# Kernel optimization log

Hardware: AMD Instinct MI355X
Metric: run time of the kernel (lower is better)

The kernel has to match this reference:

```python
import jax, jax.numpy as jnp
import numpy as np

N_NODES = 100000
N_EDGES = 1600000
D_IN = 128
D_H = 128          # hidden_channels * heads (heads=1)
N_LAYERS = 5
N_GRAPHS = 64
N_TARGETS = 1
EPS = 1e-5
NEG_SLOPE = 0.2    # PyG GATConv leaky_relu default


def setup_inputs() -> dict:
    key = jax.random.key(0)
    ks = jax.random.split(key, 16)
    x = jax.random.normal(ks[0], (N_NODES, D_IN), dtype=jnp.float32)
    edge_index = jax.random.randint(ks[1], (2, N_EDGES), 0, N_NODES, dtype=jnp.int32)
    batch = jnp.sort(jax.random.randint(ks[2], (N_NODES,), 0, N_GRAPHS, dtype=jnp.int32))
    s = 1.0 / np.sqrt(D_H)
    W = jax.random.normal(ks[3], (N_LAYERS, D_IN, D_H), dtype=jnp.float32) * s
    a_src = jax.random.normal(ks[4], (N_LAYERS, D_H), dtype=jnp.float32) * s
    a_dst = jax.random.normal(ks[5], (N_LAYERS, D_H), dtype=jnp.float32) * s
    b = jax.random.normal(ks[6], (N_LAYERS, D_H), dtype=jnp.float32) * 0.01
    bn_gamma = jnp.ones((N_LAYERS, D_H), dtype=jnp.float32) + 0.1 * jax.random.normal(ks[7], (N_LAYERS, D_H), dtype=jnp.float32)
    bn_beta = 0.1 * jax.random.normal(ks[8], (N_LAYERS, D_H), dtype=jnp.float32)
    bn_mean = 0.1 * jax.random.normal(ks[9], (N_LAYERS, D_H), dtype=jnp.float32)
    bn_var = jax.random.uniform(ks[10], (N_LAYERS, D_H), dtype=jnp.float32, minval=0.5, maxval=1.5)
    lin_w = jax.random.normal(ks[11], (D_H, N_TARGETS), dtype=jnp.float32) * s
    lin_b = jnp.zeros((N_TARGETS,), dtype=jnp.float32)
    return {"x": x, "edge_index": edge_index, "batch": batch, "W": W,
            "a_src": a_src, "a_dst": a_dst, "b": b,
            "bn_gamma": bn_gamma, "bn_beta": bn_beta, "bn_mean": bn_mean,
            "bn_var": bn_var, "lin_w": lin_w, "lin_b": lin_b}


def _gat_layer(h, src, dst, W, a_s, a_d, bias):
    # PyG GATConv (heads=1): linear transform, per-edge attention, softmax over
    # incoming edges of each destination node, weighted sum aggregation.
    xp = h @ W                                   # [N, C]
    s_node = xp @ a_s                            # [N]
    d_node = xp @ a_d                            # [N]
    e = jax.nn.leaky_relu(s_node[src] + d_node[dst], NEG_SLOPE)   # [E]
    m = jax.ops.segment_max(e, dst, num_segments=N_NODES)         # [N]
    w = jnp.exp(e - m[dst])                                       # [E]
    denom = jax.ops.segment_sum(w, dst, num_segments=N_NODES)     # [N] (>0: self-loops)
    alpha = w / denom[dst]                                        # [E]
    out = jax.ops.segment_sum(alpha[:, None] * xp[src], dst, num_segments=N_NODES)
    return out + bias


def reference(x, edge_index, batch, W, a_src, a_dst, b,
              bn_gamma, bn_beta, bn_mean, bn_var, lin_w, lin_b):
    # add self-loops (PyG GATConv default add_self_loops=True)
    loops = jnp.arange(N_NODES, dtype=edge_index.dtype)
    src = jnp.concatenate([edge_index[0], loops])
    dst = jnp.concatenate([edge_index[1], loops])
    h = x
    for l in range(N_LAYERS):
        h = _gat_layer(h, src, dst, W[l], a_src[l], a_dst[l], b[l])
        h = jax.nn.relu(h)
        # dropout: identity (eval mode); BatchNorm1d in eval mode (running stats)
        h = (h - bn_mean[l]) * (bn_gamma[l] / jnp.sqrt(bn_var[l] + EPS)) + bn_beta[l]
    # global mean pool over graphs
    sums = jax.ops.segment_sum(h, batch, num_segments=N_GRAPHS)            # [G, C]
    cnt = jax.ops.segment_sum(jnp.ones((N_NODES,), h.dtype), batch, num_segments=N_GRAPHS)
    g = sums / jnp.maximum(cnt, 1.0)[:, None]
    return g @ lin_w + lin_b
```

## Files before the change

### kernel.cpp

```cpp
#include <hip/hip_runtime.h>
#include <hip/hip_fp16.h>
#include <math.h>


#define NN 100000
#define NE 1600000
#define DH 128
#define NL 5
#define NG 64

static constexpr int ET = NE + NN;
static constexpr int NBK = (NN + 255) >> 8;
static constexpr int CAP = 6144;

typedef __attribute__((ext_vector_type(8))) _Float16 f16x8;
typedef __attribute__((ext_vector_type(4))) float f32x4;
typedef __attribute__((ext_vector_type(2))) float f32x2;

__device__ __forceinline__ unsigned short f2h(float v) {
    __half h = __float2half(v);
    return *reinterpret_cast<unsigned short*>(&h);
}
__device__ __forceinline__ float h2f(unsigned short u) {
    __half h = *reinterpret_cast<__half*>(&u);
    return __half2float(h);
}


__global__ __launch_bounds__(256) void k_wprep(const float* __restrict__ W,
                                               unsigned short* __restrict__ wtg) {
    int i = blockIdx.x * 256 + threadIdx.x;
    if (i >= NL * DH * DH) return;
    int l = i >> 14, rem = i & 16383;
    int k = rem >> 7, c = rem & 127;
    wtg[(l << 14) + (c << 7) + k] = f2h(W[i]);
}

__global__ __launch_bounds__(256) void k_bnprep(const float* __restrict__ ga,
                                                const float* __restrict__ be,
                                                const float* __restrict__ me,
                                                const float* __restrict__ va,
                                                float* __restrict__ g2,
                                                float* __restrict__ b2) {
    int i = blockIdx.x * 256 + threadIdx.x;
    if (i < NL * DH) {
        float s = ga[i] * rsqrtf(va[i] + 1e-5f);
        g2[i] = s;
        b2[i] = be[i] - me[i] * s;
    }
}

__global__ __launch_bounds__(256) void k_cnt(const int* __restrict__ batch,
                                             int* __restrict__ cnts) {
    __shared__ int hc[NG];
    int t = threadIdx.x;
    if (t < NG) hc[t] = 0;
    __syncthreads();
    int base = blockIdx.x * 4096;
#pragma unroll
    for (int k = 0; k < 16; ++k) {
        int i = base + k * 256 + t;
        if (i < NN) atomicAdd(&hc[batch[i]], 1);
    }
    __syncthreads();
    if (t < NG && hc[t]) atomicAdd(&cnts[t], hc[t]);
}


__global__ __launch_bounds__(512) void k_bscatter(const int* __restrict__ src,
                                                  const int* __restrict__ dst,
                                                  int* __restrict__ bcnt,
                                                  int* __restrict__ pairs) {
    __shared__ int lcnt[NBK];
    __shared__ int lbase[NBK];
    for (int i = threadIdx.x; i < NBK; i += 512) lcnt[i] = 0;
    __syncthreads();
    int base = blockIdx.x * 4096;
    int es[8], ed[8], er[8];
#pragma unroll
    for (int k = 0; k < 8; ++k) {
        int i = base + k * 512 + threadIdx.x;
        if (i < ET) {
            int s, d;
            if (i < NE) { s = src[i]; d = dst[i]; } else { s = d = i - NE; }
            es[k] = s; ed[k] = d;
            er[k] = atomicAdd(&lcnt[d >> 8], 1);
        } else {
            ed[k] = -1;
        }
    }
    __syncthreads();
    for (int i = threadIdx.x; i < NBK; i += 512)
        lbase[i] = lcnt[i] ? atomicAdd(&bcnt[i], lcnt[i]) : 0;
    __syncthreads();
#pragma unroll
    for (int k = 0; k < 8; ++k) {
        if (ed[k] >= 0) {
            int bk = ed[k] >> 8;
            pairs[(size_t)bk * CAP + lbase[bk] + er[k]] =
                es[k] | ((ed[k] & 255) << 17);
        }
    }
}

__global__ __launch_bounds__(512) void k_bscan(const int* __restrict__ bcnt,
                                               int* __restrict__ bbase,
                                               int* __restrict__ row_ptr) {
    __shared__ int sm[512];
    int t = threadIdx.x;
    int v = (t < NBK) ? bcnt[t] : 0;
    sm[t] = v;
    __syncthreads();
    for (int off = 1; off < 512; off <<= 1) {
        int u = (t >= off) ? sm[t - off] : 0;
        __syncthreads();
        sm[t] += u;
        __syncthreads();
    }
    if (t < NBK) bbase[t] = sm[t] - v;
    if (t == 0) { bbase[NBK] = ET; row_ptr[NN] = ET; }
}

__global__ __launch_bounds__(256) void k_bfinal(const int* __restrict__ pairs,
                                                const int* __restrict__ bcnt,
                                                const int* __restrict__ bbase,
                                                int* __restrict__ row_ptr,
                                                int* __restrict__ csr_src) {
    __shared__ int ldeg[256];
    __shared__ int lcur[256];
    __shared__ int sm[256];
    int b = blockIdx.x, t = threadIdx.x;
    int n0 = b << 8;
    int e0 = bbase[b];
    int cb = bcnt[b];
    const int* slab = pairs + (size_t)b * CAP;
    ldeg[t] = 0;
    __syncthreads();
    for (int j = t; j < cb; j += 256)
        atomicAdd(&ldeg[(slab[j] >> 17) & 255], 1);
    __syncthreads();
    int v = ldeg[t];
    sm[t] = v;
    __syncthreads();
    for (int off = 1; off < 256; off <<= 1) {
        int u = (t >= off) ? sm[t - off] : 0;
        __syncthreads();
        sm[t] += u;
        __syncthreads();
    }
    int excl = sm[t] - v;
    lcur[t] = excl;
    int n = n0 + t;
    if (n < NN) row_ptr[n] = e0 + excl;
    __syncthreads();
    for (int j = t; j < cb; j += 256) {
        int p = slab[j];
        int local = atomicAdd(&lcur[(p >> 17) & 255], 1);
        csr_src[e0 + local] = p & 0x1FFFF;
    }
}


template <bool F32IN>
__global__ __launch_bounds__(256) void k_gemm(const void* __restrict__ Av,
                                              const unsigned short* __restrict__ Wt,
                                              const float* __restrict__ a_s,
                                              const float* __restrict__ a_d,
                                              unsigned char* __restrict__ xq,
                                              float* __restrict__ s_node,
                                              float* __restrict__ d_node) {
    __shared__ __align__(16) char lds[32768];
    int tid = threadIdx.x;
    int w = tid >> 6, l = tid & 63;
    int row0 = blockIdx.x * 64;
    {
        int col = tid >> 1, seg = tid & 1;
        const char* srcp = (const char*)Wt + col * 256 + seg * 128;
#pragma unroll
        for (int i = 0; i < 8; ++i) {
            int off = seg * 128 + i * 16;
            *(uint4*)(lds + col * 256 + (off ^ ((col & 7) << 4))) =
                *(const uint4*)(srcp + i * 16);
        }
    }
    int arow = row0 + w * 16 + (l & 15);
    int arc = min(arow, NN - 1);
    f16x8 af[4];
    if constexpr (F32IN) {
        const float* ap = (const float*)Av + (size_t)arc * DH + ((l >> 4) << 3);
#pragma unroll
        for (int ks = 0; ks < 4; ++ks) {
            float4 u0 = *(const float4*)(ap + ks * 32);
            float4 u1 = *(const float4*)(ap + ks * 32 + 4);
            f16x8 v = {(_Float16)u0.x, (_Float16)u0.y, (_Float16)u0.z, (_Float16)u0.w,
                       (_Float16)u1.x, (_Float16)u1.y, (_Float16)u1.z, (_Float16)u1.w};
            af[ks] = v;
        }
    } else {
        const unsigned short* ap =
            (const unsigned short*)Av + (size_t)arc * DH + ((l >> 4) << 3);
#pragma unroll
        for (int ks = 0; ks < 4; ++ks)
            af[ks] = *(const f16x8*)(ap + ks * 32);
    }
    __syncthreads();

    f32x4 acc[8];
#pragma unroll
    for (int ct = 0; ct < 8; ++ct) acc[ct] = (f32x4){0.f, 0.f, 0.f, 0.f};
#pragma unroll
    for (int ct = 0; ct < 8; ++ct) {
        int col = ct * 16 + (l & 15);
        int cb = col * 256;
        int sw = (col & 7) << 4;
#pragma unroll
        for (int ks = 0; ks < 4; ++ks) {
            f16x8 bfr = *(const f16x8*)(lds + cb + ((ks * 64 + ((l >> 4) << 4)) ^ sw));
            acc[ct] = __builtin_amdgcn_mfma_f32_16x16x32_f16(af[ks], bfr, acc[ct], 0, 0, 0);
        }
    }

    float asv[8], adv[8];
#pragma unroll
    for (int ct = 0; ct < 8; ++ct) {
        asv[ct] = a_s[ct * 16 + (l & 15)];
        adv[ct] = a_d[ct * 16 + (l & 15)];
    }
    float ps[4] = {0.f, 0.f, 0.f, 0.f}, pd[4] = {0.f, 0.f, 0.f, 0.f};
#pragma unroll
    for (int ct = 0; ct < 8; ++ct)
#pragma unroll
        for (int r = 0; r < 4; ++r) {
            ps[r] = fmaf(acc[ct][r], asv[ct], ps[r]);
            pd[r] = fmaf(acc[ct][r], adv[ct], pd[r]);
        }
#pragma unroll
    for (int off = 8; off >= 1; off >>= 1)
#pragma unroll
        for (int r = 0; r < 4; ++r) {
            ps[r] += __shfl_xor(ps[r], off, 64);
            pd[r] += __shfl_xor(pd[r], off, 64);
        }
    int rbase = row0 + w * 16 + ((l >> 4) << 2);
    if ((l & 15) == 0) {
#pragma unroll
        for (int r = 0; r < 4; ++r) {
            int row = rbase + r;
            if (row < NN) { s_node[row] = ps[r]; d_node[row] = pd[r]; }
        }
    }
#pragma unroll
    for (int r = 0; r < 4; ++r) {
        int row = rbase + r;
        if (row < NN) {
            unsigned char* op = xq + (size_t)row * DH + (l & 15);
#pragma unroll
            for (int ct = 0; ct < 8; ++ct) {
                int pk = __builtin_amdgcn_cvt_pk_fp8_f32(acc[ct][r], 0.f, 0, false);
                op[ct * 16] = (unsigned char)(pk & 0xff);
            }
        }
    }
}


template <bool LAST>
__global__ __launch_bounds__(256) void k_aggr(const unsigned char* __restrict__ xq,
                                              const float* __restrict__ s_node,
                                              const float* __restrict__ d_node,
                                              const int* __restrict__ row_ptr,
                                              const int* __restrict__ csr_src,
                                              const float* __restrict__ bias,
                                              const float* __restrict__ g2,
                                              const float* __restrict__ b2,
                                              unsigned short* __restrict__ hout,
                                              const int* __restrict__ batch,
                                              float* __restrict__ sums) {
    __shared__ float2 stash[4][2][64];
    __shared__ float gacc[LAST ? DH : 1];
    int wid = threadIdx.x >> 6, lane = threadIdx.x & 63;
    int hi = lane >> 5, cl = lane & 31;
    int n = blockIdx.x * 8 + wid * 2 + hi;
    if constexpr (LAST) {
        if (threadIdx.x < DH) gacc[threadIdx.x] = 0.f;
        __syncthreads();
    }
    int s0 = row_ptr[n], s1 = row_ptr[n + 1];
    int deg = s1 - s0;
    float dn = d_node[n];

    int off0 = 0, off1 = 0;
    float e0 = -1e30f, e1 = -1e30f;
    {
        int j0 = s0 + cl;
        if (j0 < s1) {
            int s = csr_src[j0];
            off0 = s << 7;
            float t = s_node[s] + dn;
            e0 = (t >= 0.f) ? t : 0.2f * t;
        }
        int j1 = s0 + 32 + cl;
        if (j1 < s1) {
            int s = csr_src[j1];
            off1 = s << 7;
            float t = s_node[s] + dn;
            e1 = (t >= 0.f) ? t : 0.2f * t;
        }
    }
    float mx = fmaxf(e0, e1);
    for (int j = s0 + 64 + cl; j < s1; j += 32) {
        int s = csr_src[j];
        float t = s_node[s] + dn;
        t = (t >= 0.f) ? t : 0.2f * t;
        mx = fmaxf(mx, t);
    }
#pragma unroll
    for (int off = 16; off >= 1; off >>= 1)
        mx = fmaxf(mx, __shfl_xor(mx, off, 32));

    float w0 = (e0 > -1e29f) ? __expf(e0 - mx) : 0.f;
    float w1 = (e1 > -1e29f) ? __expf(e1 - mx) : 0.f;
    float denom = w0 + w1;
#pragma unroll
    for (int off = 16; off >= 1; off >>= 1)
        denom += __shfl_xor(denom, off, 32);

    stash[wid][hi][cl]      = make_float2(w0, __int_as_float(off0));
    stash[wid][hi][cl + 32] = make_float2(w1, __int_as_float(off1));

    unsigned int cl4 = (unsigned int)cl << 2;
    const char* xbase = (const char*)xq;
    float acc0 = 0.f, acc1 = 0.f, acc2 = 0.f, acc3 = 0.f;
    int cnt = min(deg, 64);
#pragma unroll 8
    for (int t = 0; t < cnt; ++t) {
        float2 p = stash[wid][hi][t];
        float w = p.x;
        unsigned int voff = (unsigned int)__float_as_int(p.y) + cl4;
        unsigned int v = *(const unsigned int*)(xbase + voff);
        f32x2 d0 = __builtin_amdgcn_cvt_pk_f32_fp8(v, false);
        f32x2 d1 = __builtin_amdgcn_cvt_pk_f32_fp8(v, true);
        acc0 = fmaf(w, d0[0], acc0);
        acc1 = fmaf(w, d0[1], acc1);
        acc2 = fmaf(w, d1[0], acc2);
        acc3 = fmaf(w, d1[1], acc3);
    }
    for (int j = s0 + 64; j < s1; ++j) {
        int s = csr_src[j];
        float t = s_node[s] + dn;
        t = (t >= 0.f) ? t : 0.2f * t;
        float w = __expf(t - mx);
        denom += w;
        unsigned int voff = ((unsigned int)s << 7) + cl4;
        unsigned int v = *(const unsigned int*)(xbase + voff);
        f32x2 d0 = __builtin_amdgcn_cvt_pk_f32_fp8(v, false);
        f32x2 d1 = __builtin_amdgcn_cvt_pk_f32_fp8(v, true);
        acc0 = fmaf(w, d0[0], acc0);
        acc1 = fmaf(w, d0[1], acc1);
        acc2 = fmaf(w, d1[0], acc2);
        acc3 = fmaf(w, d1[1], acc3);
    }

    float inv = 1.f / denom;
    int c = cl << 2;
    float4 bi = *(const float4*)(bias + c);
    float4 gg = *(const float4*)(g2 + c);
    float4 bb = *(const float4*)(b2 + c);
    float o0 = fmaxf(fmaf(acc0, inv, bi.x), 0.f) * gg.x + bb.x;
    float o1 = fmaxf(fmaf(acc1, inv, bi.y), 0.f) * gg.y + bb.y;
    float o2 = fmaxf(fmaf(acc2, inv, bi.z), 0.f) * gg.z + bb.z;
    float o3 = fmaxf(fmaf(acc3, inv, bi.w), 0.f) * gg.w + bb.w;

    if constexpr (!LAST) {
        ushort4 ov = {f2h(o0), f2h(o1), f2h(o2), f2h(o3)};
        *(ushort4*)(hout + (size_t)n * DH + c) = ov;
    } else {
        int g = batch[n];
        int g0 = batch[blockIdx.x * 8];
        if (g == g0) {
            atomicAdd(&gacc[c + 0], o0);
            atomicAdd(&gacc[c + 1], o1);
            atomicAdd(&gacc[c + 2], o2);
            atomicAdd(&gacc[c + 3], o3);
        } else {
            atomicAdd(&sums[g * DH + c + 0], o0);
            atomicAdd(&sums[g * DH + c + 1], o1);
            atomicAdd(&sums[g * DH + c + 2], o2);
            atomicAdd(&sums[g * DH + c + 3], o3);
        }
        __syncthreads();
        if (threadIdx.x < DH) {
            int g0b = batch[blockIdx.x * 8];
            atomicAdd(&sums[g0b * DH + threadIdx.x], gacc[threadIdx.x]);
        }
    }
}


__global__ __launch_bounds__(128) void k_pool2(const float* __restrict__ sums,
                                               const int* __restrict__ cnts,
                                               const float* __restrict__ lin_w,
                                               const float* __restrict__ lin_b,
                                               float* __restrict__ out) {
    __shared__ float sm[128];
    int g = blockIdx.x, c = threadIdx.x;
    float cnt = fmaxf((float)cnts[g], 1.f);
    sm[c] = (sums[g * DH + c] / cnt) * lin_w[c];
    __syncthreads();
    for (int off = 64; off >= 1; off >>= 1) {
        if (c < off) sm[c] += sm[c + off];
        __syncthreads();
    }
    if (c == 0) out[g] = sm[0] + lin_b[0];
}


extern "C" void kernel_launch(void* const* d_in, const int* in_sizes, int n_in,
                              void* d_out, int out_size, void* d_ws, size_t ws_size,
                              hipStream_t stream) {
    const float* x     = (const float*)d_in[0];
    const int*   ei    = (const int*)d_in[1];
    const int*   batch = (const int*)d_in[2];
    const float* W     = (const float*)d_in[3];
    const float* a_src = (const float*)d_in[4];
    const float* a_dst = (const float*)d_in[5];
    const float* b     = (const float*)d_in[6];
    const float* bn_g  = (const float*)d_in[7];
    const float* bn_b  = (const float*)d_in[8];
    const float* bn_m  = (const float*)d_in[9];
    const float* bn_v  = (const float*)d_in[10];
    const float* lin_w = (const float*)d_in[11];
    const float* lin_b = (const float*)d_in[12];
    float* out = (float*)d_out;

    const int* srcp = ei;
    const int* dstp = ei + NE;

    char* wsp = (char*)d_ws;
    size_t off = 0;
    auto alloc = [&](size_t bytes) -> void* {
        void* p = wsp + off;
        off = (off + bytes + 511) & ~((size_t)511);
        return p;
    };
    unsigned char*  xq  = (unsigned char*)alloc((size_t)NN * DH);
    unsigned short* hb  = (unsigned short*)alloc((size_t)NN * DH * 2);
    unsigned short* wtg = (unsigned short*)alloc((size_t)NL * DH * DH * 2);
    float* g2      = (float*)alloc((size_t)NL * DH * 4);
    float* b2      = (float*)alloc((size_t)NL * DH * 4);
    float* s_node  = (float*)alloc((size_t)NN * 4);
    float* d_node  = (float*)alloc((size_t)NN * 4);
    int*   row_ptr = (int*)alloc((size_t)(NN + 1) * 4);
    int*   csr_src = (int*)alloc((size_t)ET * 4);
    int*   pairs   = (int*)alloc((size_t)NBK * CAP * 4);
    int*   bcnt    = (int*)alloc((size_t)NBK * 4);
    int*   bbase   = (int*)alloc((size_t)(NBK + 1) * 4);
    float* sums    = (float*)alloc((size_t)NG * DH * 4);
    int*   cnts    = (int*)alloc((size_t)NG * 4);

    hipMemsetAsync(bcnt, 0, (size_t)NBK * 4, stream);
    hipMemsetAsync(sums, 0, (size_t)NG * DH * 4, stream);
    hipMemsetAsync(cnts, 0, (size_t)NG * 4, stream);

    k_wprep<<<(NL * DH * DH + 255) / 256, 256, 0, stream>>>(W, wtg);
    k_bnprep<<<(NL * DH + 255) / 256, 256, 0, stream>>>(bn_g, bn_b, bn_m, bn_v, g2, b2);
    k_cnt<<<(NN + 4095) / 4096, 256, 0, stream>>>(batch, cnts);

    k_bscatter<<<(ET + 4095) / 4096, 512, 0, stream>>>(srcp, dstp, bcnt, pairs);
    k_bscan<<<1, 512, 0, stream>>>(bcnt, bbase, row_ptr);
    k_bfinal<<<NBK, 256, 0, stream>>>(pairs, bcnt, bbase, row_ptr, csr_src);

    for (int l = 0; l < NL; ++l) {
        const void* hin = (l == 0) ? (const void*)x : (const void*)hb;
        if (l == 0)
            k_gemm<true><<<(NN + 63) / 64, 256, 0, stream>>>(
                hin, wtg + (size_t)l * DH * DH, a_src + l * DH, a_dst + l * DH,
                xq, s_node, d_node);
        else
            k_gemm<false><<<(NN + 63) / 64, 256, 0, stream>>>(
                hin, wtg + (size_t)l * DH * DH, a_src + l * DH, a_dst + l * DH,
                xq, s_node, d_node);
        if (l < NL - 1)
            k_aggr<false><<<NN / 8, 256, 0, stream>>>(
                xq, s_node, d_node, row_ptr, csr_src,
                b + l * DH, g2 + l * DH, b2 + l * DH, hb, batch, sums);
        else
            k_aggr<true><<<NN / 8, 256, 0, stream>>>(
                xq, s_node, d_node, row_ptr, csr_src,
                b + l * DH, g2 + l * DH, b2 + l * DH, hb, batch, sums);
    }

    k_pool2<<<NG, 128, 0, stream>>>(sums, cnts, lin_w, lin_b, out);
}
```

Before: 444.6 us.

## Move mean-pool out of last aggregation into separate pass; double GEMM block size

Global pooling moves out of the last-layer aggregation kernel into a new k_pool1 kernel. That kernel sums runs of same-graph nodes from the fp16 hidden buffer and issues far fewer global atomics. This removes heavy atomic contention on the small sums array. The cost is an extra launch, an extra read of the hidden output, and pooling from fp16-rounded values. Separately, the GEMM kernel now uses 512-thread blocks covering 128 rows each, with the weight-tile load remapped, to share the LDS weight staging across more rows.

Result: faster. 395.7 us (-11.0%).

```diff
diff --git a/kernel.cpp b/kernel.cpp
--- a/kernel.cpp
+++ b/kernel.cpp
@@ -162,7 +162,7 @@
 
 
 template <bool F32IN>
-__global__ __launch_bounds__(256) void k_gemm(const void* __restrict__ Av,
+__global__ __launch_bounds__(512) void k_gemm(const void* __restrict__ Av,
                                               const unsigned short* __restrict__ Wt,
                                               const float* __restrict__ a_s,
                                               const float* __restrict__ a_d,
@@ -172,13 +172,13 @@
     __shared__ __align__(16) char lds[32768];
     int tid = threadIdx.x;
     int w = tid >> 6, l = tid & 63;
-    int row0 = blockIdx.x * 64;
+    int row0 = blockIdx.x * 128;
     {
-        int col = tid >> 1, seg = tid & 1;
-        const char* srcp = (const char*)Wt + col * 256 + seg * 128;
-#pragma unroll
-        for (int i = 0; i < 8; ++i) {
-            int off = seg * 128 + i * 16;
+        int col = tid >> 2, seg = tid & 3;
+        const char* srcp = (const char*)Wt + col * 256 + seg * 64;
+#pragma unroll
+        for (int i = 0; i < 4; ++i) {
+            int off = seg * 64 + i * 16;
             *(uint4*)(lds + col * 256 + (off ^ ((col & 7) << 4))) =
                 *(const uint4*)(srcp + i * 16);
         }
@@ -264,7 +264,6 @@
 }
 
 
-template <bool LAST>
 __global__ __launch_bounds__(256) void k_aggr(const unsigned char* __restrict__ xq,
                                               const float* __restrict__ s_node,
                                               const float* __restrict__ d_node,
@@ -273,18 +272,11 @@
                                               const float* __restrict__ bias,
                                               const float* __restrict__ g2,
                                               const float* __restrict__ b2,
-                                              unsigned short* __restrict__ hout,
-                                              const int* __restrict__ batch,
-                                              float* __restrict__ sums) {
+                                              unsigned short* __restrict__ hout) {
     __shared__ float2 stash[4][2][64];
-    __shared__ float gacc[LAST ? DH : 1];
     int wid = threadIdx.x >> 6, lane = threadIdx.x & 63;
     int hi = lane >> 5, cl = lane & 31;
     int n = blockIdx.x * 8 + wid * 2 + hi;
-    if constexpr (LAST) {
-        if (threadIdx.x < DH) gacc[threadIdx.x] = 0.f;
-        __syncthreads();
-    }
     int s0 = row_ptr[n], s1 = row_ptr[n + 1];
     int deg = s1 - s0;
     float dn = d_node[n];
@@ -370,32 +362,30 @@
     float o1 = fmaxf(fmaf(acc1, inv, bi.y), 0.f) * gg.y + bb.y;
     float o2 = fmaxf(fmaf(acc2, inv, bi.z), 0.f) * gg.z + bb.z;
     float o3 = fmaxf(fmaf(acc3, inv, bi.w), 0.f) * gg.w + bb.w;
-
-    if constexpr (!LAST) {
-        ushort4 ov = {f2h(o0), f2h(o1), f2h(o2), f2h(o3)};
-        *(ushort4*)(hout + (size_t)n * DH + c) = ov;
-    } else {
+    ushort4 ov = {f2h(o0), f2h(o1), f2h(o2), f2h(o3)};
+    *(ushort4*)(hout + (size_t)n * DH + c) = ov;
+}
+
+
+__global__ __launch_bounds__(128) void k_pool1(const unsigned short* __restrict__ h,
+                                               const int* __restrict__ batch,
+                                               float* __restrict__ sums) {
+    int c = threadIdx.x;
+    int n0 = blockIdx.x * 64;
+    int n1 = min(NN, n0 + 64);
+    if (n0 >= NN) return;
+    float acc = 0.f;
+    int cur = batch[n0];
+    for (int n = n0; n < n1; ++n) {
         int g = batch[n];
-        int g0 = batch[blockIdx.x * 8];
-        if (g == g0) {
-            atomicAdd(&gacc[c + 0], o0);
-            atomicAdd(&gacc[c + 1], o1);
-            atomicAdd(&gacc[c + 2], o2);
-            atomicAdd(&gacc[c + 3], o3);
-        } else {
-            atomicAdd(&sums[g * DH + c + 0], o0);
-            atomicAdd(&sums[g * DH + c + 1], o1);
-            atomicAdd(&sums[g * DH + c + 2], o2);
-            atomicAdd(&sums[g * DH + c + 3], o3);
-        }
-        __syncthreads();
-        if (threadIdx.x < DH) {
-            int g0b = batch[blockIdx.x * 8];
-            atomicAdd(&sums[g0b * DH + threadIdx.x], gacc[threadIdx.x]);
-        }
-    }
-}
-
+        if (g != cur) {
+            atomicAdd(&sums[cur * DH + c], acc);
+            acc = 0.f; cur = g;
+        }
+        acc += h2f(h[(size_t)n * DH + c]);
+    }
+    atomicAdd(&sums[cur * DH + c], acc);
+}
 
 __global__ __launch_bounds__(128) void k_pool2(const float* __restrict__ sums,
                                                const int* __restrict__ cnts,
@@ -473,22 +463,18 @@
     for (int l = 0; l < NL; ++l) {
         const void* hin = (l == 0) ? (const void*)x : (const void*)hb;
         if (l == 0)
-            k_gemm<true><<<(NN + 63) / 64, 256, 0, stream>>>(
+            k_gemm<true><<<(NN + 127) / 128, 512, 0, stream>>>(
                 hin, wtg + (size_t)l * DH * DH, a_src + l * DH, a_dst + l * DH,
                 xq, s_node, d_node);
         else
-            k_gemm<false><<<(NN + 63) / 64, 256, 0, stream>>>(
+            k_gemm<false><<<(NN + 127) / 128, 512, 0, stream>>>(
                 hin, wtg + (size_t)l * DH * DH, a_src + l * DH, a_dst + l * DH,
                 xq, s_node, d_node);
-        if (l < NL - 1)
-            k_aggr<false><<<NN / 8, 256, 0, stream>>>(
-                xq, s_node, d_node, row_ptr, csr_src,
-                b + l * DH, g2 + l * DH, b2 + l * DH, hb, batch, sums);
-        else
-            k_aggr<true><<<NN / 8, 256, 0, stream>>>(
-                xq, s_node, d_node, row_ptr, csr_src,
-                b + l * DH, g2 + l * DH, b2 + l * DH, hb, batch, sums);
-    }
-
+        k_aggr<<<NN / 8, 256, 0, stream>>>(xq, s_node, d_node, row_ptr, csr_src,
+                                           b + l * DH, g2 + l * DH, b2 + l * DH,
+                                           hb);
+    }
+
+    k_pool1<<<(NN + 63) / 64, 128, 0, stream>>>(hb, batch, sums);
     k_pool2<<<NG, 128, 0, stream>>>(sums, cnts, lin_w, lin_b, out);
 }
```

## Merge prep kernels, fuse layer-0 GEMM with edge scatter, widen GEMM and pool blocks

Applied to the files above, without the earlier changes.

Three small prep kernels (weight transpose, batchnorm folding, graph counts) are merged into one launch dispatched by block index. The layer-0 GEMM and the edge bucket-scatter now share a single kernel, so independent work overlaps instead of running back to back. The GEMM moves to 512-thread blocks covering 128 rows each. The last aggregation layer now processes 64 nodes per block with two LDS accumulators to cut global atomics for pooling. The aim is lower launch overhead and better overlap of independent stages. The cost is a heterogeneous kernel with a larger LDS footprint, plus the pooling logic assumes each 64-node block spans at most two graphs (holds for the sorted batch).

New measurement: 448.9 us. Within noise of the previous version (+1.0%).

```diff
diff --git a/kernel.cpp b/kernel.cpp
--- a/kernel.cpp
+++ b/kernel.cpp
@@ -12,6 +12,11 @@
 static constexpr int ET = NE + NN;
 static constexpr int NBK = (NN + 255) >> 8;
 static constexpr int CAP = 6144;
+static constexpr int GB0 = (NN + 127) / 128;
+static constexpr int SBK = (ET + 4095) / 4096;
+static constexpr int PW = (NL * DH * DH) / 256;
+static constexpr int PB = (NL * DH + 255) / 256;
+static constexpr int PC = (NN + 4095) / 4096;
 
 typedef __attribute__((ext_vector_type(8))) _Float16 f16x8;
 typedef __attribute__((ext_vector_type(4))) float f32x4;
@@ -27,55 +32,158 @@
 }
 
 
-__global__ __launch_bounds__(256) void k_wprep(const float* __restrict__ W,
-                                               unsigned short* __restrict__ wtg) {
-    int i = blockIdx.x * 256 + threadIdx.x;
-    if (i >= NL * DH * DH) return;
-    int l = i >> 14, rem = i & 16383;
-    int k = rem >> 7, c = rem & 127;
-    wtg[(l << 14) + (c << 7) + k] = f2h(W[i]);
-}
-
-__global__ __launch_bounds__(256) void k_bnprep(const float* __restrict__ ga,
-                                                const float* __restrict__ be,
-                                                const float* __restrict__ me,
-                                                const float* __restrict__ va,
-                                                float* __restrict__ g2,
-                                                float* __restrict__ b2) {
-    int i = blockIdx.x * 256 + threadIdx.x;
-    if (i < NL * DH) {
-        float s = ga[i] * rsqrtf(va[i] + 1e-5f);
-        g2[i] = s;
-        b2[i] = be[i] - me[i] * s;
-    }
-}
-
-__global__ __launch_bounds__(256) void k_cnt(const int* __restrict__ batch,
-                                             int* __restrict__ cnts) {
+__global__ __launch_bounds__(256) void k_prep(const float* __restrict__ W,
+                                              unsigned short* __restrict__ wtg,
+                                              const float* __restrict__ ga,
+                                              const float* __restrict__ be,
+                                              const float* __restrict__ me,
+                                              const float* __restrict__ va,
+                                              float* __restrict__ g2,
+                                              float* __restrict__ b2,
+                                              const int* __restrict__ batch,
+                                              int* __restrict__ cnts) {
     __shared__ int hc[NG];
-    int t = threadIdx.x;
-    if (t < NG) hc[t] = 0;
-    __syncthreads();
-    int base = blockIdx.x * 4096;
-#pragma unroll
-    for (int k = 0; k < 16; ++k) {
-        int i = base + k * 256 + t;
-        if (i < NN) atomicAdd(&hc[batch[i]], 1);
-    }
-    __syncthreads();
-    if (t < NG && hc[t]) atomicAdd(&cnts[t], hc[t]);
-}
-
-
-__global__ __launch_bounds__(512) void k_bscatter(const int* __restrict__ src,
-                                                  const int* __restrict__ dst,
-                                                  int* __restrict__ bcnt,
-                                                  int* __restrict__ pairs) {
-    __shared__ int lcnt[NBK];
-    __shared__ int lbase[NBK];
+    int bid = blockIdx.x, t = threadIdx.x;
+    if (bid < PW) {
+        int i = bid * 256 + t;
+        int l = i >> 14, rem = i & 16383;
+        int k = rem >> 7, c = rem & 127;
+        wtg[(l << 14) + (c << 7) + k] = f2h(W[i]);
+    } else if (bid < PW + PB) {
+        int i = (bid - PW) * 256 + t;
+        if (i < NL * DH) {
+            float s = ga[i] * rsqrtf(va[i] + 1e-5f);
+            g2[i] = s;
+            b2[i] = be[i] - me[i] * s;
+        }
+    } else {
+        if (t < NG) hc[t] = 0;
+        __syncthreads();
+        int base = (bid - PW - PB) * 4096;
+#pragma unroll
+        for (int k = 0; k < 16; ++k) {
+            int i = base + k * 256 + t;
+            if (i < NN) atomicAdd(&hc[batch[i]], 1);
+        }
+        __syncthreads();
+        if (t < NG && hc[t]) atomicAdd(&cnts[t], hc[t]);
+    }
+}
+
+
+template <bool F32IN>
+__device__ __forceinline__ void gemm_body(char* lds, int bid,
+                                          const void* __restrict__ Av,
+                                          const unsigned short* __restrict__ Wt,
+                                          const float* __restrict__ a_s,
+                                          const float* __restrict__ a_d,
+                                          unsigned char* __restrict__ xq,
+                                          float* __restrict__ s_node,
+                                          float* __restrict__ d_node) {
+    int tid = threadIdx.x;
+    int w = tid >> 6, l = tid & 63;
+    int row0 = bid * 128;
+    {
+        int col = tid >> 2, seg = tid & 3;
+        const char* srcp = (const char*)Wt + col * 256 + seg * 64;
+#pragma unroll
+        for (int i = 0; i < 4; ++i) {
+            int off = seg * 64 + i * 16;
+            *(uint4*)(lds + col * 256 + (off ^ ((col & 7) << 4))) =
+                *(const uint4*)(srcp + i * 16);
+        }
+    }
+    int arow = row0 + w * 16 + (l & 15);
+    int arc = min(arow, NN - 1);
+    f16x8 af[4];
+    if constexpr (F32IN) {
+        const float* ap = (const float*)Av + (size_t)arc * DH + ((l >> 4) << 3);
+#pragma unroll
+        for (int ks = 0; ks < 4; ++ks) {
+            float4 u0 = *(const float4*)(ap + ks * 32);
+            float4 u1 = *(const float4*)(ap + ks * 32 + 4);
+            f16x8 v = {(_Float16)u0.x, (_Float16)u0.y, (_Float16)u0.z, (_Float16)u0.w,
+                       (_Float16)u1.x, (_Float16)u1.y, (_Float16)u1.z, (_Float16)u1.w};
+            af[ks] = v;
+        }
+    } else {
+        const unsigned short* ap =
+            (const unsigned short*)Av + (size_t)arc * DH + ((l >> 4) << 3);
+#pragma unroll
+        for (int ks = 0; ks < 4; ++ks)
+            af[ks] = *(const f16x8*)(ap + ks * 32);
+    }
+    __syncthreads();
+
+    f32x4 acc[8];
+#pragma unroll
+    for (int ct = 0; ct < 8; ++ct) acc[ct] = (f32x4){0.f, 0.f, 0.f, 0.f};
+#pragma unroll
+    for (int ct = 0; ct < 8; ++ct) {
+        int col = ct * 16 + (l & 15);
+        int cb = col * 256;
+        int sw = (col & 7) << 4;
+#pragma unroll
+        for (int ks = 0; ks < 4; ++ks) {
+            f16x8 bfr = *(const f16x8*)(lds + cb + ((ks * 64 + ((l >> 4) << 4)) ^ sw));
+            acc[ct] = __builtin_amdgcn_mfma_f32_16x16x32_f16(af[ks], bfr, acc[ct], 0, 0, 0);
+        }
+    }
+
+    float asv[8], adv[8];
+#pragma unroll
+    for (int ct = 0; ct < 8; ++ct) {
+        asv[ct] = a_s[ct * 16 + (l & 15)];
+        adv[ct] = a_d[ct * 16 + (l & 15)];
+    }
+    float ps[4] = {0.f, 0.f, 0.f, 0.f}, pd[4] = {0.f, 0.f, 0.f, 0.f};
+#pragma unroll
+    for (int ct = 0; ct < 8; ++ct)
+#pragma unroll
+        for (int r = 0; r < 4; ++r) {
+            ps[r] = fmaf(acc[ct][r], asv[ct], ps[r]);
+            pd[r] = fmaf(acc[ct][r], adv[ct], pd[r]);
+        }
+#pragma unroll
+    for (int off = 8; off >= 1; off >>= 1)
+#pragma unroll
+        for (int r = 0; r < 4; ++r) {
+            ps[r] += __shfl_xor(ps[r], off, 64);
+            pd[r] += __shfl_xor(pd[r], off, 64);
+        }
+    int rbase = row0 + w * 16 + ((l >> 4) << 2);
+    if ((l & 15) == 0) {
+#pragma unroll
+        for (int r = 0; r < 4; ++r) {
+            int row = rbase + r;
+            if (row < NN) { s_node[row] = ps[r]; d_node[row] = pd[r]; }
+        }
+    }
+#pragma unroll
+    for (int r = 0; r < 4; ++r) {
+        int row = rbase + r;
+        if (row < NN) {
+            unsigned char* op = xq + (size_t)row * DH + (l & 15);
+#pragma unroll
+            for (int ct = 0; ct < 8; ++ct) {
+                int pk = __builtin_amdgcn_cvt_pk_fp8_f32(acc[ct][r], 0.f, 0, false);
+                op[ct * 16] = (unsigned char)(pk & 0xff);
+            }
+        }
+    }
+}
+
+
+__device__ __forceinline__ void bscatter_body(char* smem, int bid,
+                                              const int* __restrict__ src,
+                                              const int* __restrict__ dst,
+                                              int* __restrict__ bcnt,
+                                              int* __restrict__ pairs) {
+    int* lcnt = (int*)smem;
+    int* lbase = lcnt + NBK;
     for (int i = threadIdx.x; i < NBK; i += 512) lcnt[i] = 0;
     __syncthreads();
-    int base = blockIdx.x * 4096;
+    int base = bid * 4096;
     int es[8], ed[8], er[8];
 #pragma unroll
     for (int k = 0; k < 8; ++k) {
@@ -102,6 +210,38 @@
         }
     }
 }
+
+
+__global__ __launch_bounds__(512) void k_mega(const float* __restrict__ x,
+                                              const unsigned short* __restrict__ Wt,
+                                              const float* __restrict__ a_s,
+                                              const float* __restrict__ a_d,
+                                              unsigned char* __restrict__ xq,
+                                              float* __restrict__ s_node,
+                                              float* __restrict__ d_node,
+                                              const int* __restrict__ src,
+                                              const int* __restrict__ dst,
+                                              int* __restrict__ bcnt,
+                                              int* __restrict__ pairs) {
+    __shared__ __align__(16) char smem[35904];
+    if (blockIdx.x < GB0)
+        gemm_body<true>(smem, blockIdx.x, x, Wt, a_s, a_d, xq, s_node, d_node);
+    else
+        bscatter_body(smem, blockIdx.x - GB0, src, dst, bcnt, pairs);
+}
+
+
+__global__ __launch_bounds__(512) void k_gemm(const unsigned short* __restrict__ A,
+                                              const unsigned short* __restrict__ Wt,
+                                              const float* __restrict__ a_s,
+                                              const float* __restrict__ a_d,
+                                              unsigned char* __restrict__ xq,
+                                              float* __restrict__ s_node,
+                                              float* __restrict__ d_node) {
+    __shared__ __align__(16) char lds[32768];
+    gemm_body<false>(lds, blockIdx.x, A, Wt, a_s, a_d, xq, s_node, d_node);
+}
+
 
 __global__ __launch_bounds__(512) void k_bscan(const int* __restrict__ bcnt,
                                                int* __restrict__ bbase,
@@ -161,109 +301,6 @@
 }
 
 
-template <bool F32IN>
-__global__ __launch_bounds__(256) void k_gemm(const void* __restrict__ Av,
-                                              const unsigned short* __restrict__ Wt,
-                                              const float* __restrict__ a_s,
-                                              const float* __restrict__ a_d,
-                                              unsigned char* __restrict__ xq,
-                                              float* __restrict__ s_node,
-                                              float* __restrict__ d_node) {
-    __shared__ __align__(16) char lds[32768];
-    int tid = threadIdx.x;
-    int w = tid >> 6, l = tid & 63;
-    int row0 = blockIdx.x * 64;
-    {
-        int col = tid >> 1, seg = tid & 1;
-        const char* srcp = (const char*)Wt + col * 256 + seg * 128;
-#pragma unroll
-        for (int i = 0; i < 8; ++i) {
-            int off = seg * 128 + i * 16;
-            *(uint4*)(lds + col * 256 + (off ^ ((col & 7) << 4))) =
-                *(const uint4*)(srcp + i * 16);
-        }
-    }
-    int arow = row0 + w * 16 + (l & 15);
-    int arc = min(arow, NN - 1);
-    f16x8 af[4];
-    if constexpr (F32IN) {
-        const float* ap = (const float*)Av + (size_t)arc * DH + ((l >> 4) << 3);
-#pragma unroll
-        for (int ks = 0; ks < 4; ++ks) {
-            float4 u0 = *(const float4*)(ap + ks * 32);
-            float4 u1 = *(const float4*)(ap + ks * 32 + 4);
-            f16x8 v = {(_Float16)u0.x, (_Float16)u0.y, (_Float16)u0.z, (_Float16)u0.w,
-                       (_Float16)u1.x, (_Float16)u1.y, (_Float16)u1.z, (_Float16)u1.w};
-            af[ks] = v;
-        }
-    } else {
-        const unsigned short* ap =
-            (const unsigned short*)Av + (size_t)arc * DH + ((l >> 4) << 3);
-#pragma unroll
-        for (int ks = 0; ks < 4; ++ks)
-            af[ks] = *(const f16x8*)(ap + ks * 32);
-    }
-    __syncthreads();
-
-    f32x4 acc[8];
-#pragma unroll
-    for (int ct = 0; ct < 8; ++ct) acc[ct] = (f32x4){0.f, 0.f, 0.f, 0.f};
-#pragma unroll
-    for (int ct = 0; ct < 8; ++ct) {
-        int col = ct * 16 + (l & 15);
-        int cb = col * 256;
-        int sw = (col & 7) << 4;
-#pragma unroll
-        for (int ks = 0; ks < 4; ++ks) {
-            f16x8 bfr = *(const f16x8*)(lds + cb + ((ks * 64 + ((l >> 4) << 4)) ^ sw));
-            acc[ct] = __builtin_amdgcn_mfma_f32_16x16x32_f16(af[ks], bfr, acc[ct], 0, 0, 0);
-        }
-    }
-
-    float asv[8], adv[8];
-#pragma unroll
-    for (int ct = 0; ct < 8; ++ct) {
-        asv[ct] = a_s[ct * 16 + (l & 15)];
-        adv[ct] = a_d[ct * 16 + (l & 15)];
-    }
-    float ps[4] = {0.f, 0.f, 0.f, 0.f}, pd[4] = {0.f, 0.f, 0.f, 0.f};
-#pragma unroll
-    for (int ct = 0; ct < 8; ++ct)
-#pragma unroll
-        for (int r = 0; r < 4; ++r) {
-            ps[r] = fmaf(acc[ct][r], asv[ct], ps[r]);
-            pd[r] = fmaf(acc[ct][r], adv[ct], pd[r]);
-        }
-#pragma unroll
-    for (int off = 8; off >= 1; off >>= 1)
-#pragma unroll
-        for (int r = 0; r < 4; ++r) {
-            ps[r] += __shfl_xor(ps[r], off, 64);
-            pd[r] += __shfl_xor(pd[r], off, 64);
-        }
-    int rbase = row0 + w * 16 + ((l >> 4) << 2);
-    if ((l & 15) == 0) {
-#pragma unroll
-        for (int r = 0; r < 4; ++r) {
-            int row = rbase + r;
-            if (row < NN) { s_node[row] = ps[r]; d_node[row] = pd[r]; }
-        }
-    }
-#pragma unroll
-    for (int r = 0; r < 4; ++r) {
-        int row = rbase + r;
-        if (row < NN) {
-            unsigned char* op = xq + (size_t)row * DH + (l & 15);
-#pragma unroll
-            for (int ct = 0; ct < 8; ++ct) {
-                int pk = __builtin_amdgcn_cvt_pk_fp8_f32(acc[ct][r], 0.f, 0, false);
-                op[ct * 16] = (unsigned char)(pk & 0xff);
-            }
-        }
-    }
-}
-
-
 template <bool LAST>
 __global__ __launch_bounds__(256) void k_aggr(const unsigned char* __restrict__ xq,
                                               const float* __restrict__ s_node,
@@ -277,121 +314,128 @@
                                               const int* __restrict__ batch,
                                               float* __restrict__ sums) {
     __shared__ float2 stash[4][2][64];
-    __shared__ float gacc[LAST ? DH : 1];
+    __shared__ float gacc[LAST ? 256 : 1];
     int wid = threadIdx.x >> 6, lane = threadIdx.x & 63;
     int hi = lane >> 5, cl = lane & 31;
-    int n = blockIdx.x * 8 + wid * 2 + hi;
+    int g0 = 0, g1 = 0;
     if constexpr (LAST) {
-        if (threadIdx.x < DH) gacc[threadIdx.x] = 0.f;
-        __syncthreads();
-    }
-    int s0 = row_ptr[n], s1 = row_ptr[n + 1];
-    int deg = s1 - s0;
-    float dn = d_node[n];
-
-    int off0 = 0, off1 = 0;
-    float e0 = -1e30f, e1 = -1e30f;
-    {
-        int j0 = s0 + cl;
-        if (j0 < s1) {
-            int s = csr_src[j0];
-            off0 = s << 7;
-            float t = s_node[s] + dn;
-            e0 = (t >= 0.f) ? t : 0.2f * t;
-        }
-        int j1 = s0 + 32 + cl;
-        if (j1 < s1) {
-            int s = csr_src[j1];
-            off1 = s << 7;
-            float t = s_node[s] + dn;
-            e1 = (t >= 0.f) ? t : 0.2f * t;
-        }
-    }
-    float mx = fmaxf(e0, e1);
-    for (int j = s0 + 64 + cl; j < s1; j += 32) {
-        int s = csr_src[j];
-        float t = s_node[s] + dn;
-        t = (t >= 0.f) ? t : 0.2f * t;
-        mx = fmaxf(mx, t);
-    }
-#pragma unroll
-    for (int off = 16; off >= 1; off >>= 1)
-        mx = fmaxf(mx, __shfl_xor(mx, off, 32));
-
-    float w0 = (e0 > -1e29f) ? __expf(e0 - mx) : 0.f;
-    float w1 = (e1 > -1e29f) ? __expf(e1 - mx) : 0.f;
-    float denom = w0 + w1;
-#pragma unroll
-    for (int off = 16; off >= 1; off >>= 1)
-        denom += __shfl_xor(denom, off, 32);
-
-    stash[wid][hi][cl]      = make_float2(w0, __int_as_float(off0));
-    stash[wid][hi][cl + 32] = make_float2(w1, __int_as_float(off1));
-
-    unsigned int cl4 = (unsigned int)cl << 2;
-    const char* xbase = (const char*)xq;
-    float acc0 = 0.f, acc1 = 0.f, acc2 = 0.f, acc3 = 0.f;
-    int cnt = min(deg, 64);
+        int first = (int)blockIdx.x * 64;
+        int last = first + 63;
+        if (last > NN - 1) last = NN - 1;
+        g0 = batch[first];
+        g1 = batch[last];
+        gacc[threadIdx.x] = 0.f;
+        __syncthreads();
+    }
+    const int rounds = LAST ? 8 : 1;
+    for (int it = 0; it < rounds; ++it) {
+        int n = LAST ? ((int)blockIdx.x * 64 + it * 8 + wid * 2 + hi)
+                     : ((int)blockIdx.x * 8 + wid * 2 + hi);
+        if (!LAST || n < NN) {
+            int s0 = row_ptr[n], s1 = row_ptr[n + 1];
+            int deg = s1 - s0;
+            float dn = d_node[n];
+
+            int off0 = 0, off1 = 0;
+            float e0 = -1e30f, e1 = -1e30f;
+            {
+                int j0 = s0 + cl;
+                if (j0 < s1) {
+                    int s = csr_src[j0];
+                    off0 = s << 7;
+                    float t = s_node[s] + dn;
+                    e0 = (t >= 0.f) ? t : 0.2f * t;
+                }
+                int j1 = s0 + 32 + cl;
+                if (j1 < s1) {
+                    int s = csr_src[j1];
+                    off1 = s << 7;
+                    float t = s_node[s] + dn;
+                    e1 = (t >= 0.f) ? t : 0.2f * t;
+                }
+            }
+            float mx = fmaxf(e0, e1);
+            for (int j = s0 + 64 + cl; j < s1; j += 32) {
+                int s = csr_src[j];
+                float t = s_node[s] + dn;
+                t = (t >= 0.f) ? t : 0.2f * t;
+                mx = fmaxf(mx, t);
+            }
+#pragma unroll
+            for (int off = 16; off >= 1; off >>= 1)
+                mx = fmaxf(mx, __shfl_xor(mx, off, 32));
+
+            float w0 = (e0 > -1e29f) ? __expf(e0 - mx) : 0.f;
+            float w1 = (e1 > -1e29f) ? __expf(e1 - mx) : 0.f;
+            float denom = w0 + w1;
+#pragma unroll
+            for (int off = 16; off >= 1; off >>= 1)
+                denom += __shfl_xor(denom, off, 32);
+
+            stash[wid][hi][cl]      = make_float2(w0, __int_as_float(off0));
+            stash[wid][hi][cl + 32] = make_float2(w1, __int_as_float(off1));
+
+            unsigned int cl4 = (unsigned int)cl << 2;
+            const char* xbase = (const char*)xq;
+            float acc0 = 0.f, acc1 = 0.f, acc2 = 0.f, acc3 = 0.f;
+            int cnt = min(deg, 64);
 #pragma unroll 8
-    for (int t = 0; t < cnt; ++t) {
-        float2 p = stash[wid][hi][t];
-        float w = p.x;
-        unsigned int voff = (unsigned int)__float_as_int(p.y) + cl4;
-        unsigned int v = *(const unsigned int*)(xbase + voff);
-        f32x2 d0 = __builtin_amdgcn_cvt_pk_f32_fp8(v, false);
-        f32x2 d1 = __builtin_amdgcn_cvt_pk_f32_fp8(v, true);
-        acc0 = fmaf(w, d0[0], acc0);
-        acc1 = fmaf(w, d0[1], acc1);
-        acc2 = fmaf(w, d1[0], acc2);
-        acc3 = fmaf(w, d1[1], acc3);
-    }
-    for (int j = s0 + 64; j < s1; ++j) {
-        int s = csr_src[j];
-        float t = s_node[s] + dn;
-        t = (t >= 0.f) ? t : 0.2f * t;
-        float w = __expf(t - mx);
-        denom += w;
-        unsigned int voff = ((unsigned int)s << 7) + cl4;
-        unsigned int v = *(const unsigned int*)(xbase + voff);
-        f32x2 d0 = __builtin_amdgcn_cvt_pk_f32_fp8(v, false);
-        f32x2 d1 = __builtin_amdgcn_cvt_pk_f32_fp8(v, true);
-        acc0 = fmaf(w, d0[0], acc0);
-        acc1 = fmaf(w, d0[1], acc1);
-        acc2 = fmaf(w, d1[0], acc2);
-        acc3 = fmaf(w, d1[1], acc3);
-    }
-
-    float inv = 1.f / denom;
-    int c = cl << 2;
-    float4 bi = *(const float4*)(bias + c);
-    float4 gg = *(const float4*)(g2 + c);
-    float4 bb = *(const float4*)(b2 + c);
-    float o0 = fmaxf(fmaf(acc0, inv, bi.x), 0.f) * gg.x + bb.x;
-    float o1 = fmaxf(fmaf(acc1, inv, bi.y), 0.f) * gg.y + bb.y;
-    float o2 = fmaxf(fmaf(acc2, inv, bi.z), 0.f) * gg.z + bb.z;
-    float o3 = fmaxf(fmaf(acc3, inv, bi.w), 0.f) * gg.w + bb.w;
-
-    if constexpr (!LAST) {
-        ushort4 ov = {f2h(o0), f2h(o1), f2h(o2), f2h(o3)};
-        *(ushort4*)(hout + (size_t)n * DH + c) = ov;
-    } else {
-        int g = batch[n];
-        int g0 = batch[blockIdx.x * 8];
-        if (g == g0) {
-            atomicAdd(&gacc[c + 0], o0);
-            atomicAdd(&gacc[c + 1], o1);
-            atomicAdd(&gacc[c + 2], o2);
-            atomicAdd(&gacc[c + 3], o3);
-        } else {
-            atomicAdd(&sums[g * DH + c + 0], o0);
-            atomicAdd(&sums[g * DH + c + 1], o1);
-            atomicAdd(&sums[g * DH + c + 2], o2);
-            atomicAdd(&sums[g * DH + c + 3], o3);
-        }
+            for (int t = 0; t < cnt; ++t) {
+                float2 p = stash[wid][hi][t];
+                float w = p.x;
+                unsigned int voff = (unsigned int)__float_as_int(p.y) + cl4;
+                unsigned int v = *(const unsigned int*)(xbase + voff);
+                f32x2 d0 = __builtin_amdgcn_cvt_pk_f32_fp8(v, false);
+                f32x2 d1 = __builtin_amdgcn_cvt_pk_f32_fp8(v, true);
+                acc0 = fmaf(w, d0[0], acc0);
+                acc1 = fmaf(w, d0[1], acc1);
+                acc2 = fmaf(w, d1[0], acc2);
+                acc3 = fmaf(w, d1[1], acc3);
+            }
+            for (int j = s0 + 64; j < s1; ++j) {
+                int s = csr_src[j];
+                float t = s_node[s] + dn;
+                t = (t >= 0.f) ? t : 0.2f * t;
+                float w = __expf(t - mx);
+                denom += w;
+                unsigned int voff = ((unsigned int)s << 7) + cl4;
+                unsigned int v = *(const unsigned int*)(xbase + voff);
+                f32x2 d0 = __builtin_amdgcn_cvt_pk_f32_fp8(v, false);
+                f32x2 d1 = __builtin_amdgcn_cvt_pk_f32_fp8(v, true);
+                acc0 = fmaf(w, d0[0], acc0);
+                acc1 = fmaf(w, d0[1], acc1);
+                acc2 = fmaf(w, d1[0], acc2);
+                acc3 = fmaf(w, d1[1], acc3);
+            }
+
+            float inv = 1.f / denom;
+            int c = cl << 2;
+            float4 bi = *(const float4*)(bias + c);
+            float4 gg = *(const float4*)(g2 + c);
+            float4 bb = *(const float4*)(b2 + c);
+            float o0 = fmaxf(fmaf(acc0, inv, bi.x), 0.f) * gg.x + bb.x;
+            float o1 = fmaxf(fmaf(acc1, inv, bi.y), 0.f) * gg.y + bb.y;
+            float o2 = fmaxf(fmaf(acc2, inv, bi.z), 0.f) * gg.z + bb.z;
+            float o3 = fmaxf(fmaf(acc3, inv, bi.w), 0.f) * gg.w + bb.w;
+
+            if constexpr (!LAST) {
+                ushort4 ov = {f2h(o0), f2h(o1), f2h(o2), f2h(o3)};
+                *(ushort4*)(hout + (size_t)n * DH + c) = ov;
+            } else {
+                int slot = (batch[n] != g0) ? 128 : 0;
+                atomicAdd(&gacc[slot + c + 0], o0);
+                atomicAdd(&gacc[slot + c + 1], o1);
+                atomicAdd(&gacc[slot + c + 2], o2);
+                atomicAdd(&gacc[slot + c + 3], o3);
+            }
+        }
+    }
+    if constexpr (LAST) {
         __syncthreads();
         if (threadIdx.x < DH) {
-            int g0b = batch[blockIdx.x * 8];
-            atomicAdd(&sums[g0b * DH + threadIdx.x], gacc[threadIdx.x]);
+            atomicAdd(&sums[g0 * DH + threadIdx.x], gacc[threadIdx.x]);
+            if (g1 != g0)
+                atomicAdd(&sums[g1 * DH + threadIdx.x], gacc[128 + threadIdx.x]);
         }
     }
 }
@@ -458,34 +502,29 @@
     float* sums    = (float*)alloc((size_t)NG * DH * 4);
     int*   cnts    = (int*)alloc((size_t)NG * 4);
 
-    hipMemsetAsync(bcnt, 0, (size_t)NBK * 4, stream);
-    hipMemsetAsync(sums, 0, (size_t)NG * DH * 4, stream);
-    hipMemsetAsync(cnts, 0, (size_t)NG * 4, stream);
-
-    k_wprep<<<(NL * DH * DH + 255) / 256, 256, 0, stream>>>(W, wtg);
-    k_bnprep<<<(NL * DH + 255) / 256, 256, 0, stream>>>(bn_g, bn_b, bn_m, bn_v, g2, b2);
-    k_cnt<<<(NN + 4095) / 4096, 256, 0, stream>>>(batch, cnts);
-
-    k_bscatter<<<(ET + 4095) / 4096, 512, 0, stream>>>(srcp, dstp, bcnt, pairs);
+    hipError_t e0_ = hipMemsetAsync(bcnt, 0, (size_t)NBK * 4, stream); (void)e0_;
+    hipError_t e1_ = hipMemsetAsync(sums, 0, (size_t)NG * DH * 4, stream); (void)e1_;
+    hipError_t e2_ = hipMemsetAsync(cnts, 0, (size_t)NG * 4, stream); (void)e2_;
+
+    k_prep<<<PW + PB + PC, 256, 0, stream>>>(W, wtg, bn_g, bn_b, bn_m, bn_v,
+                                             g2, b2, batch, cnts);
+
+    k_mega<<<GB0 + SBK, 512, 0, stream>>>(x, wtg, a_src, a_dst, xq,
+                                          s_node, d_node, srcp, dstp, bcnt, pairs);
     k_bscan<<<1, 512, 0, stream>>>(bcnt, bbase, row_ptr);
     k_bfinal<<<NBK, 256, 0, stream>>>(pairs, bcnt, bbase, row_ptr, csr_src);
 
     for (int l = 0; l < NL; ++l) {
-        const void* hin = (l == 0) ? (const void*)x : (const void*)hb;
-        if (l == 0)
-            k_gemm<true><<<(NN + 63) / 64, 256, 0, stream>>>(
-                hin, wtg + (size_t)l * DH * DH, a_src + l * DH, a_dst + l * DH,
-                xq, s_node, d_node);
-        else
-            k_gemm<false><<<(NN + 63) / 64, 256, 0, stream>>>(
-                hin, wtg + (size_t)l * DH * DH, a_src + l * DH, a_dst + l * DH,
-                xq, s_node, d_node);
+        if (l > 0)
+            k_gemm<<<GB0, 512, 0, stream>>>(hb, wtg + (size_t)l * DH * DH,
+                                            a_src + l * DH, a_dst + l * DH,
+                                            xq, s_node, d_node);
         if (l < NL - 1)
             k_aggr<false><<<NN / 8, 256, 0, stream>>>(
                 xq, s_node, d_node, row_ptr, csr_src,
                 b + l * DH, g2 + l * DH, b2 + l * DH, hb, batch, sums);
         else
-            k_aggr<true><<<NN / 8, 256, 0, stream>>>(
+            k_aggr<true><<<(NN + 63) / 64, 256, 0, stream>>>(
                 xq, s_node, d_node, row_ptr, csr_src,
                 b + l * DH, g2 + l * DH, b2 + l * DH, hb, batch, sums);
     }
```
